# Performance work log

Hardware: AMD Instinct MI355X
Metric: run time of the kernel (lower is better)

## Reference

```python
import jax, jax.numpy as jnp
import numpy as np

B, S, D, H = 2, 2048, 1024, 16
DH = D // H


def setup_inputs() -> dict:
    key = jax.random.key(0)
    ks = jax.random.split(key, 5)
    scale = 0.02
    return {
        "X": jax.random.normal(ks[0], (B, S, D), jnp.float32),
        "Wq": jax.random.normal(ks[1], (H, D, DH), jnp.float32) * scale,
        "Wk": jax.random.normal(ks[2], (H, D, DH), jnp.float32) * scale,
        "Wv": jax.random.normal(ks[3], (H, D, DH), jnp.float32) * scale,
        "Wo": jax.random.normal(ks[4], (D, D), jnp.float32) * scale,
        "bo": jnp.zeros((D,), jnp.float32),
    }


def reference(X, Wq, Wk, Wv, Wo, bo):
    # Per-head projections, batched over heads: [B,H,S,DH]
    Q = jnp.einsum('bsd,hde->bhse', X, Wq)
    K = jnp.einsum('bsd,hde->bhse', X, Wk)
    V = jnp.einsum('bsd,hde->bhse', X, Wv)
    # Scores scaled by sqrt(d_model) exactly as in the source (not sqrt(d_head))
    A = jnp.einsum('bhse,bhte->bhst', Q, K) / jnp.sqrt(jnp.float32(D))
    A = jax.nn.softmax(A, axis=-1)  # no mask in the source
    O = jnp.einsum('bhst,bhte->bhse', A, V)  # [B,H,S,DH]
    # Concat heads -> [B,S,D], then output projection
    O = jnp.transpose(O, (0, 2, 1, 3)).reshape(B, S, D)
    return O @ Wo + bo
```

## Files before the change

kernel.cpp:

```cpp
#include <hip/hip_runtime.h>
#include <math.h>

static constexpr int Bc  = 2;
static constexpr int Sc  = 2048;
static constexpr int Dc  = 1024;
static constexpr int Hc  = 16;
static constexpr int DHc = 64;

typedef short bf16x8 __attribute__((ext_vector_type(8)));
typedef float f32x4  __attribute__((ext_vector_type(4)));

static constexpr float LOG2E = 1.4426950408889634f;

static __device__ __forceinline__ unsigned short f2bf(float x) {
  union { float f; unsigned u; } v; v.f = x;
  unsigned r = v.u + 0x7FFFu + ((v.u >> 16) & 1u);
  return (unsigned short)(r >> 16);
}
static __device__ __forceinline__ float bf2f(unsigned short u) {
  union { unsigned u; float f; } v; v.u = ((unsigned)u) << 16;
  return v.f;
}
static __device__ __forceinline__ unsigned pk2bf_trunc(float a, float b) {
  return __builtin_amdgcn_perm(__float_as_uint(b), __float_as_uint(a), 0x07060302u);
}
#if __has_builtin(__builtin_amdgcn_exp2f)
#define EXP2F(x) __builtin_amdgcn_exp2f(x)
#else
#define EXP2F(x) exp2f(x)
#endif

static __device__ __forceinline__ void gload16(const void* g, void* l) {
  __builtin_amdgcn_global_load_lds(
      (const __attribute__((address_space(1))) void*)g,
      (__attribute__((address_space(3))) void*)l, 16, 0, 0);
}

__global__ __launch_bounds__(256) void prep(
    const float* __restrict__ Wq, const float* __restrict__ Wk,
    const float* __restrict__ Wv, const float* __restrict__ Wo,
    const float* __restrict__ X,
    unsigned short* __restrict__ Wt3, unsigned short* __restrict__ Wot,
    unsigned short* __restrict__ Xb) {
  const int z = blockIdx.z;
  if (z == 4) {
    size_t base = ((size_t)blockIdx.y * 16 + blockIdx.x) * 4096;
#pragma unroll
    for (int it = 0; it < 16; ++it) {
      size_t i = base + it * 256 + threadIdx.x;
      float4 v = ((const float4*)X)[i];
      ushort4 u; u.x = f2bf(v.x); u.y = f2bf(v.y); u.z = f2bf(v.z); u.w = f2bf(v.w);
      ((ushort4*)Xb)[i] = u;
    }
    return;
  }
  __shared__ unsigned short T[64][68];
  const float* src; unsigned short* dst;
  int srcld, dstld, r0, c0;
  if (z < 3) {
    const float* W = (z == 0) ? Wq : (z == 1) ? Wk : Wv;
    unsigned short* Wt = Wt3 + (size_t)z * Dc * Dc;
    int h = blockIdx.y;
    src = W + (size_t)h * Dc * DHc;  srcld = DHc; r0 = blockIdx.x * 64; c0 = 0;
    dst = Wt + (size_t)h * DHc * Dc; dstld = Dc;
  } else {
    src = Wo;  srcld = Dc; r0 = blockIdx.x * 64; c0 = blockIdx.y * 64;
    dst = Wot; dstld = Dc;
  }
#pragma unroll
  for (int it = 0; it < 16; ++it) {
    int idx = it * 256 + threadIdx.x;
    int r = idx >> 6, c = idx & 63;
    T[c][r] = f2bf(src[(size_t)(r0 + r) * srcld + c0 + c]);
  }
  __syncthreads();
#pragma unroll
  for (int it = 0; it < 4; ++it) {
    int idx = it * 256 + threadIdx.x;
    int c = idx >> 4, r4 = (idx & 15) * 4;
    ushort4 u = *(const ushort4*)&T[c][r4];
    *(ushort4*)&dst[(size_t)(c0 + c) * dstld + r0 + r4] = u;
  }
}

__global__ __launch_bounds__(512, 2) void qkv_gemm(
    const unsigned short* __restrict__ Xb, const unsigned short* __restrict__ Wt3,
    unsigned short* __restrict__ Qb, unsigned short* __restrict__ Kb,
    unsigned short* __restrict__ Vtb) {
  __shared__ alignas(16) unsigned char smem[135168];
  unsigned short (*S)[64] = (unsigned short(*)[64])smem;

  const int tid = threadIdx.x;
  const int wv = tid >> 6, lane = tid & 63;
  const int ln = lane & 15, qd = (lane >> 4) & 3;
  const int wm = wv >> 2, wn = wv & 3;
  const int lr = lane >> 3;
  const int gcol = ((lane & 7) ^ lr) * 8;
  const int paq = ln & 7;

  const int bid = blockIdx.x;
  const int l = (bid & 7) * 24 + (bid >> 3);
  const int xb = l & 15, y = l >> 4;
  const int m0 = xb * 256, n0 = y * 256;
  const int which = y >> 2;
  const int b = m0 >> 11, s0 = m0 & 2047;
  const int h0 = (y & 3) * 4;

  const unsigned short* Ap = Xb + (size_t)m0 * 1024;
  const unsigned short* Bp = Wt3 + (size_t)n0 * 1024;
  const int grow = wv * 16 + lr;

#define STG(gb, srow) do {                                                  \
    gload16((gb) + (size_t)grow * 1024 + gcol,       &S[(srow) + wv * 16][0]); \
    gload16((gb) + (size_t)(grow + 8) * 1024 + gcol, &S[(srow) + wv * 16 + 8][0]); \
  } while (0)

#define RD_A(mh, rowbase) do {                                              \
    _Pragma("unroll") for (int mt = 0; mt < 4; ++mt)                        \
      _Pragma("unroll") for (int ks = 0; ks < 2; ++ks)                      \
        af[mt][ks] = *(const bf16x8*)&S[(rowbase) + (mh) * 64 + mt * 16 + ln] \
                                       [((ks * 4 + qd) ^ paq) * 8];         \
  } while (0)

#define RD_B(nh, rowbase) do {                                              \
    _Pragma("unroll") for (int nt = 0; nt < 2; ++nt)                        \
      _Pragma("unroll") for (int ks = 0; ks < 2; ++ks)                      \
        bf[(nh) * 2 + nt][ks] = *(const bf16x8*)&S[(rowbase) + (nh) * 32 + nt * 16 + ln] \
                                                  [((ks * 4 + qd) ^ paq) * 8]; \
  } while (0)

#define MM(mh, nh) do {                                                     \
    _Pragma("unroll") for (int ks = 0; ks < 2; ++ks)                        \
      _Pragma("unroll") for (int mt = 0; mt < 4; ++mt)                      \
        _Pragma("unroll") for (int nt = 0; nt < 2; ++nt)                    \
          acc[(mh) * 4 + mt][(nh) * 2 + nt] =                               \
              __builtin_amdgcn_mfma_f32_16x16x32_bf16(                      \
                  af[mt][ks], bf[(nh) * 2 + nt][ks],                        \
                  acc[(mh) * 4 + mt][(nh) * 2 + nt], 0, 0, 0);              \
  } while (0)

#define BAR __builtin_amdgcn_s_barrier()
#define WAITL asm volatile("s_waitcnt lgkmcnt(0)" ::: "memory")
#define WAITV(n) asm volatile("s_waitcnt vmcnt(" #n ")" ::: "memory")
#define PRIO1 __builtin_amdgcn_s_setprio(1)
#define PRIO0 __builtin_amdgcn_s_setprio(0)

  f32x4 acc[8][4];
#pragma unroll
  for (int mt = 0; mt < 8; ++mt)
#pragma unroll
    for (int nt = 0; nt < 4; ++nt) acc[mt][nt] = (f32x4){0.f, 0.f, 0.f, 0.f};

  STG(Bp, 512);
  STG(Ap, 0);
  STG(Ap + 128 * 1024, 128);
  STG(Bp + 128 * 1024, 640);
  STG(Bp + 64, 768);
  STG(Ap + 64, 256);
  WAITV(4);
  BAR;

  bf16x8 af[4][2], bf[4][2];

  for (int j = 0; j < 8; ++j) {
    const int last = (j == 7);
    const unsigned short* Ak = Ap + j * 128;
    const unsigned short* Bk = Bp + j * 128;

    STG(Ak + 128 * 1024 + 64, 384);
    RD_A(0, wm * 128);
    RD_B(0, 512 + (wn >> 1) * 128 + (wn & 1) * 64);
    BAR; WAITL;
    PRIO1; MM(0, 0); PRIO0; BAR;
    STG(Bk + 128 * 1024 + 64, 896);
    RD_B(1, 512 + (wn >> 1) * 128 + (wn & 1) * 64);
    BAR; WAITL;
    PRIO1; MM(0, 1); PRIO0; BAR;
    if (!last) STG(Bk + 128, 512);
    RD_A(1, wm * 128);
    BAR; WAITL;
    PRIO1; MM(1, 0); PRIO0; BAR;
    if (!last) STG(Ak + 128, 0);
    BAR;
    PRIO1; MM(1, 1); PRIO0;
    if (last) { WAITV(0); } else { WAITV(4); }
    BAR;

    if (!last) STG(Ak + 128 * 1024 + 128, 128);
    RD_A(0, 256 + wm * 128);
    RD_B(0, 768 + (wn >> 1) * 128 + (wn & 1) * 64);
    BAR; WAITL;
    PRIO1; MM(0, 0); PRIO0; BAR;
    if (!last) STG(Bk + 128 * 1024 + 128, 640);
    RD_B(1, 768 + (wn >> 1) * 128 + (wn & 1) * 64);
    BAR; WAITL;
    PRIO1; MM(0, 1); PRIO0; BAR;
    if (!last) STG(Bk + 192, 768);
    RD_A(1, 256 + wm * 128);
    BAR; WAITL;
    PRIO1; MM(1, 0); PRIO0; BAR;
    if (!last) STG(Ak + 192, 256);
    BAR;
    PRIO1; MM(1, 1); PRIO0;
    if (!last) WAITV(4);
    BAR;
  }

  unsigned short* Ts = (unsigned short*)smem;
  if (which < 2) {
    unsigned short* Out = (which == 0) ? Qb : Kb;
    const float scale = (which == 0) ? (LOG2E / 32.0f) : 1.0f;
#pragma unroll
    for (int mt = 0; mt < 8; ++mt)
#pragma unroll
      for (int nt = 0; nt < 4; ++nt)
#pragma unroll
        for (int r = 0; r < 4; ++r)
          Ts[(wm * 128 + mt * 16 + qd * 4 + r) * 264 + wn * 64 + nt * 16 + ln] =
              f2bf(acc[mt][nt][r] * scale);
    __syncthreads();
    const int row = tid >> 1;
#pragma unroll
    for (int it = 0; it < 16; ++it) {
      int c16 = (tid & 1) * 16 + it;
      int head = c16 >> 3, e8 = c16 & 7;
      *(ulonglong2*)&Out[(((size_t)b * Hc + h0 + head) * Sc + s0 + row) * DHc + e8 * 8] =
          *(const ulonglong2*)&Ts[row * 264 + c16 * 8];
    }
  } else {
#pragma unroll
    for (int mt = 0; mt < 8; ++mt)
#pragma unroll
      for (int nt = 0; nt < 4; ++nt)
#pragma unroll
        for (int r = 0; r < 4; ++r)
          Ts[(wn * 64 + nt * 16 + ln) * 264 + wm * 128 + mt * 16 + qd * 4 + r] =
              f2bf(acc[mt][nt][r]);
    __syncthreads();
    const int n = tid >> 1;
    const int head = n >> 6, e = n & 63;
    unsigned short* dst = Vtb + (((size_t)b * Hc + h0 + head) * DHc + e) * Sc + s0;
#pragma unroll
    for (int it = 0; it < 16; ++it) {
      int s16 = (tid & 1) * 16 + it;
      *(ulonglong2*)&dst[s16 * 8] = *(const ulonglong2*)&Ts[n * 264 + s16 * 8];
    }
  }
#undef STG
#undef RD_A
#undef RD_B
#undef MM
#undef BAR
#undef WAITL
#undef WAITV
#undef PRIO1
#undef PRIO0
}

__global__ __launch_bounds__(256, 2) void attn_partial(
    const unsigned short* __restrict__ Qb, const unsigned short* __restrict__ Kb,
    const unsigned short* __restrict__ Vtb,
    unsigned short* __restrict__ Opart, float* __restrict__ lpart) {
  __shared__ alignas(16) unsigned short Ks[2][64][64];
  __shared__ alignas(16) unsigned short Vts[2][64][64];
  __shared__ alignas(16) unsigned short Ps[256][64];

  const int tid = threadIdx.x;
  const int wv = tid >> 6, lane = tid & 63;
  const int ln = tid & 15, qd = (tid >> 4) & 3;
  const int l0 = blockIdx.x + 8 * blockIdx.y + 256 * blockIdx.z;
  const int wid = (l0 & 7) * 64 + (l0 >> 3);
  const int sT = wid & 7, bh = (wid >> 3) & 31, sp = wid >> 8;
  const int lr = lane >> 3;
  const int lcs = ((lane & 7) ^ lr) * 8;

#define ABAR __builtin_amdgcn_s_barrier()
#define AWAITV0 asm volatile("s_waitcnt vmcnt(0)" ::: "memory")
#define APRIO1 __builtin_amdgcn_s_setprio(1)
#define APRIO0 __builtin_amdgcn_s_setprio(0)

  bf16x8 qf[4][2];
  const size_t qrow0 = (size_t)bh * Sc + sT * 256 + wv * 64;
#pragma unroll
  for (int mt = 0; mt < 4; ++mt)
#pragma unroll
    for (int ks = 0; ks < 2; ++ks)
      qf[mt][ks] = *(const bf16x8*)&Qb[(qrow0 + mt * 16 + ln) * DHc + ks * 32 + qd * 8];

  bf16x8 vones;
#pragma unroll
  for (int j = 0; j < 8; ++j) vones[j] = (short)0x3F80;

  f32x4 o[4][4], lacc[4];
#pragma unroll
  for (int mt = 0; mt < 4; ++mt) {
    lacc[mt] = (f32x4){0.f, 0.f, 0.f, 0.f};
#pragma unroll
    for (int et = 0; et < 4; ++et) o[mt][et] = (f32x4){0.f, 0.f, 0.f, 0.f};
  }

#define ASTG(kb, buf) do {                                                   \
    _Pragma("unroll") for (int t = 0; t < 2; ++t) {                          \
      gload16(Kb + ((size_t)bh * Sc + (kb) * 64 + wv * 16 + t * 8 + lr) * DHc + lcs, \
              &Ks[(buf)][wv * 16 + t * 8][0]);                               \
      gload16(Vtb + ((size_t)bh * DHc + wv * 16 + t * 8 + lr) * Sc + (kb) * 64 + lcs, \
              &Vts[(buf)][wv * 16 + t * 8][0]);                              \
    }                                                                        \
  } while (0)

  ASTG(sp * 16, 0);
  AWAITV0;
  ABAR;

#pragma unroll 2
  for (int i = 0; i < 16; ++i) {
    const int kb = sp * 16 + i;
    const int cur = i & 1;
    if (i < 15) ASTG(kb + 1, cur ^ 1);

    f32x4 st[4][4];
#pragma unroll
    for (int mt = 0; mt < 4; ++mt)
#pragma unroll
      for (int nt = 0; nt < 4; ++nt) st[mt][nt] = (f32x4){0.f, 0.f, 0.f, 0.f};
#pragma unroll
    for (int ks = 0; ks < 2; ++ks) {
      const int pa = ((ks * 4 + qd) ^ (ln & 7)) * 8;
#pragma unroll
      for (int nt = 0; nt < 4; ++nt) {
        bf16x8 kf = *(const bf16x8*)&Ks[cur][nt * 16 + ln][pa];
        APRIO1;
#pragma unroll
        for (int mt = 0; mt < 4; ++mt)
          st[mt][nt] = __builtin_amdgcn_mfma_f32_16x16x32_bf16(kf, qf[mt][ks], st[mt][nt], 0, 0, 0);
        APRIO0;
      }
    }

#pragma unroll
    for (int mt = 0; mt < 4; ++mt) {
      const int prow = wv * 64 + mt * 16 + ln;
#pragma unroll
      for (int nt = 0; nt < 4; ++nt) {
        float p0 = EXP2F(st[mt][nt][0]);
        float p1 = EXP2F(st[mt][nt][1]);
        float p2 = EXP2F(st[mt][nt][2]);
        float p3 = EXP2F(st[mt][nt][3]);
        uint2 w;
        w.x = pk2bf_trunc(p0, p1);
        w.y = pk2bf_trunc(p2, p3);
        int ppos = ((2 * nt + (qd >> 1)) ^ (ln & 7)) * 8 + (qd & 1) * 4;
        *(uint2*)&Ps[prow][ppos] = w;
      }
    }

#pragma unroll
    for (int ks = 0; ks < 2; ++ks) {
      const int pa = ((ks * 4 + qd) ^ (ln & 7)) * 8;
      bf16x8 pf[4];
#pragma unroll
      for (int mt = 0; mt < 4; ++mt) {
        pf[mt] = *(const bf16x8*)&Ps[wv * 64 + mt * 16 + ln][pa];
        lacc[mt] = __builtin_amdgcn_mfma_f32_16x16x32_bf16(pf[mt], vones, lacc[mt], 0, 0, 0);
      }
#pragma unroll
      for (int et = 0; et < 4; ++et) {
        bf16x8 vf = *(const bf16x8*)&Vts[cur][et * 16 + ln][pa];
        APRIO1;
#pragma unroll
        for (int mt = 0; mt < 4; ++mt)
          o[mt][et] = __builtin_amdgcn_mfma_f32_16x16x32_bf16(pf[mt], vf, o[mt][et], 0, 0, 0);
        APRIO0;
      }
    }

    AWAITV0;
    ABAR;
  }

  const size_t pbase = (size_t)sp * 65536 + ((size_t)bh * 8 + sT) * 256;
  if (ln == 0) {
#pragma unroll
    for (int mt = 0; mt < 4; ++mt)
#pragma unroll
      for (int r = 0; r < 4; ++r)
        lpart[pbase + wv * 64 + mt * 16 + qd * 4 + r] = lacc[mt][r];
  }
#pragma unroll
  for (int mt = 0; mt < 4; ++mt)
#pragma unroll
    for (int r = 0; r < 4; ++r) {
      int row = wv * 64 + mt * 16 + qd * 4 + r;
#pragma unroll
      for (int et = 0; et < 4; ++et)
        Opart[(pbase + row) * DHc + et * 16 + ln] = f2bf(o[mt][et][r]);
    }
#undef ASTG
#undef ABAR
#undef AWAITV0
#undef APRIO1
#undef APRIO0
}

__global__ __launch_bounds__(256) void combine(
    const unsigned short* __restrict__ Opart, const float* __restrict__ lpart,
    unsigned short* __restrict__ Ocat) {
  const int sT = blockIdx.x, bh = blockIdx.y, tid = threadIdx.x;
  const int b = bh >> 4, h = bh & 15;
  const size_t p0 = ((size_t)bh * 8 + sT) * 256;
  const size_t p1 = p0 + 65536;
#pragma unroll
  for (int it = 0; it < 16; ++it) {
    int idx = it * 256 + tid;
    int row = idx >> 4, c4 = (idx & 15) * 4;
    ushort4 u0 = *(const ushort4*)&Opart[(p0 + row) * DHc + c4];
    ushort4 u1 = *(const ushort4*)&Opart[(p1 + row) * DHc + c4];
    float inv = 1.0f / (lpart[p0 + row] + lpart[p1 + row]);
    ushort4 w;
    w.x = f2bf((bf2f(u0.x) + bf2f(u1.x)) * inv);
    w.y = f2bf((bf2f(u0.y) + bf2f(u1.y)) * inv);
    w.z = f2bf((bf2f(u0.z) + bf2f(u1.z)) * inv);
    w.w = f2bf((bf2f(u0.w) + bf2f(u1.w)) * inv);
    *(ushort4*)&Ocat[((size_t)b * Sc + sT * 256 + row) * Dc + h * DHc + c4] = w;
  }
}

__global__ __launch_bounds__(256) void out_gemm(
    const unsigned short* __restrict__ Ab, const unsigned short* __restrict__ Wot,
    const float* __restrict__ bo, float* __restrict__ Out) {
  __shared__ alignas(16) unsigned short As[64][64];
  __shared__ alignas(16) unsigned short Bs[128][64];

  const int tid = threadIdx.x;
  const int wv = tid >> 6, lane = tid & 63;
  const int ln = tid & 15, qd = (tid >> 4) & 3;
  const int wm = wv >> 1, wn = wv & 1;
  const int m0 = blockIdx.x * 64, n0 = blockIdx.y * 128;
  const int lr = lane >> 3;
  const int lcs = ((lane & 7) ^ lr) * 8;

  f32x4 acc[2][4];
#pragma unroll
  for (int mt = 0; mt < 2; ++mt)
#pragma unroll
    for (int nt = 0; nt < 4; ++nt) acc[mt][nt] = (f32x4){0.f, 0.f, 0.f, 0.f};

  for (int k0 = 0; k0 < Dc; k0 += 64) {
    __syncthreads();
#pragma unroll
    for (int t = 0; t < 2; ++t)
      gload16(Ab + (size_t)(m0 + wv * 16 + t * 8 + lr) * Dc + k0 + lcs, &As[wv * 16 + t * 8][0]);
#pragma unroll
    for (int t = 0; t < 4; ++t)
      gload16(Wot + (size_t)(n0 + wv * 32 + t * 8 + lr) * Dc + k0 + lcs, &Bs[wv * 32 + t * 8][0]);
    __syncthreads();
#pragma unroll
    for (int ks = 0; ks < 2; ++ks) {
      const int pa = ((ks * 4 + qd) ^ (ln & 7)) * 8;
      bf16x8 af[2], bf[4];
#pragma unroll
      for (int mt = 0; mt < 2; ++mt)
        af[mt] = *(const bf16x8*)&As[wm * 32 + mt * 16 + ln][pa];
#pragma unroll
      for (int nt = 0; nt < 4; ++nt)
        bf[nt] = *(const bf16x8*)&Bs[wn * 64 + nt * 16 + ln][pa];
#pragma unroll
      for (int mt = 0; mt < 2; ++mt)
#pragma unroll
        for (int nt = 0; nt < 4; ++nt)
          acc[mt][nt] = __builtin_amdgcn_mfma_f32_16x16x32_bf16(af[mt], bf[nt], acc[mt][nt], 0, 0, 0);
    }
  }

  float bias[4];
#pragma unroll
  for (int nt = 0; nt < 4; ++nt) bias[nt] = bo[n0 + wn * 64 + nt * 16 + ln];

#pragma unroll
  for (int mt = 0; mt < 2; ++mt)
#pragma unroll
    for (int r = 0; r < 4; ++r) {
      int m = m0 + wm * 32 + mt * 16 + qd * 4 + r;
#pragma unroll
      for (int nt = 0; nt < 4; ++nt)
        Out[(size_t)m * Dc + n0 + wn * 64 + nt * 16 + ln] = acc[mt][nt][r] + bias[nt];
    }
}

extern "C" void kernel_launch(void* const* d_in, const int* in_sizes, int n_in,
                              void* d_out, int out_size, void* d_ws, size_t ws_size,
                              hipStream_t stream) {
  (void)in_sizes; (void)n_in; (void)out_size; (void)ws_size;
  const float* X  = (const float*)d_in[0];
  const float* Wq = (const float*)d_in[1];
  const float* Wk = (const float*)d_in[2];
  const float* Wv = (const float*)d_in[3];
  const float* Wo = (const float*)d_in[4];
  const float* bo = (const float*)d_in[5];
  float* out = (float*)d_out;

  const size_t nX = (size_t)Bc * Sc * Dc;
  unsigned short* Xb    = (unsigned short*)d_ws;
  unsigned short* Wt3   = Xb + nX;
  unsigned short* Wot   = Wt3 + (size_t)3 * Dc * Dc;
  unsigned short* Qb    = Wot + (size_t)Dc * Dc;
  unsigned short* Kb    = Qb + nX;
  unsigned short* Vtb   = Kb + nX;
  unsigned short* Opart = Vtb + nX;
  float* lpart = (float*)(Opart + 2 * nX);
  unsigned short* Ocat = Xb;

  prep<<<dim3(16, 16, 5), 256, 0, stream>>>(Wq, Wk, Wv, Wo, X, Wt3, Wot, Xb);
  qkv_gemm<<<dim3(192), 512, 0, stream>>>(Xb, Wt3, Qb, Kb, Vtb);
  attn_partial<<<dim3(8, 32, 2), 256, 0, stream>>>(Qb, Kb, Vtb, Opart, lpart);
  combine<<<dim3(8, 32), 256, 0, stream>>>(Opart, lpart, Ocat);
  out_gemm<<<dim3(64, 8), 256, 0, stream>>>(Ocat, Wot, bo, out);
}
```

Before: 185.8 us.

## Software-pipeline attention loop: overlap next QK^T with current softmax and PV

Restructures the attention inner loop so the QK^T scores for block i+1 are computed while block i's exp/pack and PV MMAs run. K and V loads are split and issued separately, with loads running two blocks ahead and partial vmcnt waits in place of full drains. This hides load latency and exp latency behind MFMA work, at the cost of a second score register array, which adds register pressure at 2 waves per SIMD.

```diff
diff --git a/kernel.cpp b/kernel.cpp
--- a/kernel.cpp
+++ b/kernel.cpp
@@ -275,7 +275,7 @@
   const int lcs = ((lane & 7) ^ lr) * 8;
 
 #define ABAR __builtin_amdgcn_s_barrier()
-#define AWAITV0 asm volatile("s_waitcnt vmcnt(0)" ::: "memory")
+#define AWAITV(n) asm volatile("s_waitcnt vmcnt(" #n ")" ::: "memory")
 #define APRIO1 __builtin_amdgcn_s_setprio(1)
 #define APRIO0 __builtin_amdgcn_s_setprio(0)
 
@@ -299,84 +299,99 @@
     for (int et = 0; et < 4; ++et) o[mt][et] = (f32x4){0.f, 0.f, 0.f, 0.f};
   }
 
-#define ASTG(kb, buf) do {                                                   \
-    _Pragma("unroll") for (int t = 0; t < 2; ++t) {                          \
+#define ASTG_K(kb, buf) do {                                                 \
+    _Pragma("unroll") for (int t = 0; t < 2; ++t)                            \
       gload16(Kb + ((size_t)bh * Sc + (kb) * 64 + wv * 16 + t * 8 + lr) * DHc + lcs, \
               &Ks[(buf)][wv * 16 + t * 8][0]);                               \
+  } while (0)
+#define ASTG_V(kb, buf) do {                                                 \
+    _Pragma("unroll") for (int t = 0; t < 2; ++t)                            \
       gload16(Vtb + ((size_t)bh * DHc + wv * 16 + t * 8 + lr) * Sc + (kb) * 64 + lcs, \
               &Vts[(buf)][wv * 16 + t * 8][0]);                              \
+  } while (0)
+
+#define QK_INTO(SN, kbuf) do {                                               \
+    _Pragma("unroll") for (int mt = 0; mt < 4; ++mt)                         \
+      _Pragma("unroll") for (int nt = 0; nt < 4; ++nt)                       \
+        SN[mt][nt] = (f32x4){0.f, 0.f, 0.f, 0.f};                            \
+    _Pragma("unroll") for (int ks = 0; ks < 2; ++ks) {                       \
+      const int pa = ((ks * 4 + qd) ^ (ln & 7)) * 8;                         \
+      _Pragma("unroll") for (int nt = 0; nt < 4; ++nt) {                     \
+        bf16x8 kf = *(const bf16x8*)&Ks[(kbuf)][nt * 16 + ln][pa];           \
+        _Pragma("unroll") for (int mt = 0; mt < 4; ++mt)                     \
+          SN[mt][nt] = __builtin_amdgcn_mfma_f32_16x16x32_bf16(              \
+              kf, qf[mt][ks], SN[mt][nt], 0, 0, 0);                          \
+      }                                                                      \
     }                                                                        \
   } while (0)
 
-  ASTG(sp * 16, 0);
-  AWAITV0;
+#define EXPPACK(SC) do {                                                     \
+    _Pragma("unroll") for (int mt = 0; mt < 4; ++mt) {                       \
+      const int prow = wv * 64 + mt * 16 + ln;                               \
+      _Pragma("unroll") for (int nt = 0; nt < 4; ++nt) {                     \
+        float p0 = EXP2F(SC[mt][nt][0]);                                     \
+        float p1 = EXP2F(SC[mt][nt][1]);                                     \
+        float p2 = EXP2F(SC[mt][nt][2]);                                     \
+        float p3 = EXP2F(SC[mt][nt][3]);                                     \
+        uint2 w;                                                             \
+        w.x = pk2bf_trunc(p0, p1);                                           \
+        w.y = pk2bf_trunc(p2, p3);                                           \
+        int ppos = ((2 * nt + (qd >> 1)) ^ (ln & 7)) * 8 + (qd & 1) * 4;     \
+        *(uint2*)&Ps[prow][ppos] = w;                                        \
+      }                                                                      \
+    }                                                                        \
+  } while (0)
+
+#define PV(vbuf) do {                                                        \
+    _Pragma("unroll") for (int ks = 0; ks < 2; ++ks) {                       \
+      const int pa = ((ks * 4 + qd) ^ (ln & 7)) * 8;                         \
+      bf16x8 pf[4];                                                          \
+      _Pragma("unroll") for (int mt = 0; mt < 4; ++mt) {                     \
+        pf[mt] = *(const bf16x8*)&Ps[wv * 64 + mt * 16 + ln][pa];            \
+        lacc[mt] = __builtin_amdgcn_mfma_f32_16x16x32_bf16(pf[mt], vones,    \
+                                                           lacc[mt], 0, 0, 0); \
+      }                                                                      \
+      APRIO1;                                                                \
+      _Pragma("unroll") for (int et = 0; et < 4; ++et) {                     \
+        bf16x8 vf = *(const bf16x8*)&Vts[(vbuf)][et * 16 + ln][pa];          \
+        _Pragma("unroll") for (int mt = 0; mt < 4; ++mt)                     \
+          o[mt][et] = __builtin_amdgcn_mfma_f32_16x16x32_bf16(pf[mt], vf,    \
+                                                              o[mt][et], 0, 0, 0); \
+      }                                                                      \
+      APRIO0;                                                                \
+    }                                                                        \
+  } while (0)
+
+#define BODY(i_, SC, SN, DO_NEXT, DO_STG, WV)                                \
+  {                                                                          \
+    AWAITV(WV);                       \
+    ABAR;                        \
+    if (DO_STG) ASTG_K(sp * 16 + (i_) + 2, (i_) & 1);                        \
+    if (DO_NEXT) QK_INTO(SN, ((i_) + 1) & 1);                                \
+    EXPPACK(SC);                    \
+    PV((i_) & 1);                                                            \
+    ABAR;                               \
+    if (DO_STG) ASTG_V(sp * 16 + (i_) + 2, (i_) & 1);                        \
+  }
+
+  f32x4 stA[4][4], stB[4][4];
+
+  ASTG_K(sp * 16 + 0, 0);
+  ASTG_V(sp * 16 + 0, 0);
+  ASTG_K(sp * 16 + 1, 1);
+  AWAITV(4);
   ABAR;
-
-#pragma unroll 2
-  for (int i = 0; i < 16; ++i) {
-    const int kb = sp * 16 + i;
-    const int cur = i & 1;
-    if (i < 15) ASTG(kb + 1, cur ^ 1);
-
-    f32x4 st[4][4];
-#pragma unroll
-    for (int mt = 0; mt < 4; ++mt)
-#pragma unroll
-      for (int nt = 0; nt < 4; ++nt) st[mt][nt] = (f32x4){0.f, 0.f, 0.f, 0.f};
-#pragma unroll
-    for (int ks = 0; ks < 2; ++ks) {
-      const int pa = ((ks * 4 + qd) ^ (ln & 7)) * 8;
-#pragma unroll
-      for (int nt = 0; nt < 4; ++nt) {
-        bf16x8 kf = *(const bf16x8*)&Ks[cur][nt * 16 + ln][pa];
-        APRIO1;
-#pragma unroll
-        for (int mt = 0; mt < 4; ++mt)
-          st[mt][nt] = __builtin_amdgcn_mfma_f32_16x16x32_bf16(kf, qf[mt][ks], st[mt][nt], 0, 0, 0);
-        APRIO0;
-      }
-    }
-
-#pragma unroll
-    for (int mt = 0; mt < 4; ++mt) {
-      const int prow = wv * 64 + mt * 16 + ln;
-#pragma unroll
-      for (int nt = 0; nt < 4; ++nt) {
-        float p0 = EXP2F(st[mt][nt][0]);
-        float p1 = EXP2F(st[mt][nt][1]);
-        float p2 = EXP2F(st[mt][nt][2]);
-        float p3 = EXP2F(st[mt][nt][3]);
-        uint2 w;
-        w.x = pk2bf_trunc(p0, p1);
-        w.y = pk2bf_trunc(p2, p3);
-        int ppos = ((2 * nt + (qd >> 1)) ^ (ln & 7)) * 8 + (qd & 1) * 4;
-        *(uint2*)&Ps[prow][ppos] = w;
-      }
-    }
-
-#pragma unroll
-    for (int ks = 0; ks < 2; ++ks) {
-      const int pa = ((ks * 4 + qd) ^ (ln & 7)) * 8;
-      bf16x8 pf[4];
-#pragma unroll
-      for (int mt = 0; mt < 4; ++mt) {
-        pf[mt] = *(const bf16x8*)&Ps[wv * 64 + mt * 16 + ln][pa];
-        lacc[mt] = __builtin_amdgcn_mfma_f32_16x16x32_bf16(pf[mt], vones, lacc[mt], 0, 0, 0);
-      }
-#pragma unroll
-      for (int et = 0; et < 4; ++et) {
-        bf16x8 vf = *(const bf16x8*)&Vts[cur][et * 16 + ln][pa];
-        APRIO1;
-#pragma unroll
-        for (int mt = 0; mt < 4; ++mt)
-          o[mt][et] = __builtin_amdgcn_mfma_f32_16x16x32_bf16(pf[mt], vf, o[mt][et], 0, 0, 0);
-        APRIO0;
-      }
-    }
-
-    AWAITV0;
-    ABAR;
-  }
+  QK_INTO(stA, 0);
+  ASTG_V(sp * 16 + 1, 1);
+
+#pragma unroll 1
+  for (int j = 0; j < 7; ++j) {
+    const int i0 = 2 * j;
+    BODY(i0,     stA, stB, 1, 1, 2)
+    BODY(i0 + 1, stB, stA, 1, 1, 2)
+  }
+  BODY(14, stA, stB, 1, 0, 0)
+  BODY(15, stB, stA, 0, 0, 0)
 
   const size_t pbase = (size_t)sp * 65536 + ((size_t)bh * 8 + sT) * 256;
   if (ln == 0) {
@@ -395,9 +410,14 @@
       for (int et = 0; et < 4; ++et)
         Opart[(pbase + row) * DHc + et * 16 + ln] = f2bf(o[mt][et][r]);
     }
-#undef ASTG
+#undef ASTG_K
+#undef ASTG_V
+#undef QK_INTO
+#undef EXPPACK
+#undef PV
+#undef BODY
 #undef ABAR
-#undef AWAITV0
+#undef AWAITV
 #undef APRIO1
 #undef APRIO0
 }
```

Result: slower. 247.6 us (+33.3%).
